# Kernel optimization log

Measured on AMD Instinct MI355X. Metric: run time of the kernel, lower is better.

Reference implementation:

```python
import jax, jax.numpy as jnp
import numpy as np

N = 50000
E = 800000
H = 2          # heads
C = 64         # out channels per head (embedding_size)
NEG_SLOPE = 0.2


def setup_inputs() -> dict:
    key = jax.random.key(0)
    ks = jax.random.split(key, 8)
    x = jax.random.normal(ks[0], (N, 1), dtype=jnp.float32)
    edge_index = jax.random.randint(ks[1], (2, E), 0, N, dtype=jnp.int64)
    edge_attr = jax.random.normal(ks[2], (E, 1), dtype=jnp.float32)
    # GATv2Conv params: lin_l, lin_r (with bias), lin_edge (no bias), att, out bias
    W_l = jax.random.normal(ks[3], (1, H * C), dtype=jnp.float32)
    b_l = jnp.zeros((H * C,), dtype=jnp.float32)
    W_r = jax.random.normal(ks[4], (1, H * C), dtype=jnp.float32)
    b_r = jnp.zeros((H * C,), dtype=jnp.float32)
    W_e = jax.random.normal(ks[5], (1, H * C), dtype=jnp.float32)
    att = jax.random.normal(ks[6], (H, C), dtype=jnp.float32)
    bias = jnp.zeros((H * C,), dtype=jnp.float32)
    return {"x": x, "edge_index": edge_index, "edge_attr": edge_attr,
            "W_l": W_l, "b_l": b_l, "W_r": W_r, "b_r": b_r,
            "W_e": W_e, "att": att, "bias": bias}


def reference(x, edge_index, edge_attr, W_l, b_l, W_r, b_r, W_e, att, bias):
    n = x.shape[0]
    src, dst = edge_index[0], edge_index[1]

    # add_self_loops=True with fill_value='mean': self-loop edge_attr at node i
    # is the mean of incoming edge_attr (0 if no incoming edges).
    attr_sum = jax.ops.segment_sum(edge_attr, dst, num_segments=n)      # [N,1]
    cnt = jax.ops.segment_sum(jnp.ones((src.shape[0], 1), edge_attr.dtype), dst, num_segments=n)
    loop_attr = attr_sum / jnp.maximum(cnt, 1.0)                         # [N,1]

    loop = jnp.arange(n, dtype=src.dtype)
    src_f = jnp.concatenate([src, loop])                                 # [E+N]
    dst_f = jnp.concatenate([dst, loop])
    attr_f = jnp.concatenate([edge_attr, loop_attr], axis=0)             # [E+N,1]

    x_l = (x @ W_l + b_l).reshape(n, H, C)    # source transform
    x_r = (x @ W_r + b_r).reshape(n, H, C)    # target transform
    e = (attr_f @ W_e).reshape(-1, H, C)      # edge feature embedding

    # GATv2 attention: leaky_relu(x_l[j] + x_r[i] + e) . att
    g = jax.nn.leaky_relu(x_l[src_f] + x_r[dst_f] + e, NEG_SLOPE)        # [E+N,H,C]
    logits = jnp.einsum('ehc,hc->eh', g, att)                            # [E+N,H]

    # segment softmax grouped by destination node
    mx = jax.ops.segment_max(logits, dst_f, num_segments=n)              # [N,H]
    a = jnp.exp(logits - mx[dst_f])
    den = jax.ops.segment_sum(a, dst_f, num_segments=n)                  # [N,H]
    alpha = a / den[dst_f]                                               # [E+N,H]

    # weighted scatter-add of source messages
    out = jax.ops.segment_sum(alpha[:, :, None] * x_l[src_f], dst_f, num_segments=n)  # [N,H,C]
    return out.reshape(n, H * C) + bias
```

## Files before the change

kernel.cpp:

```cpp
#include <hip/hip_runtime.h>

#define NEG 0.2f

typedef float f4v __attribute__((ext_vector_type(4)));

__device__ __forceinline__ float leaky(float v){ return fmaxf(v, NEG * v); }

__global__ void __launch_bounds__(256) k_edge(
        const int* __restrict__ src, const int* __restrict__ dst,
        const float* __restrict__ attr, const float* __restrict__ x,
        const float* __restrict__ Wl, const float* __restrict__ Wr,
        const float* __restrict__ We, const float* __restrict__ bl,
        const float* __restrict__ br, const float* __restrict__ att,
        int* __restrict__ head4, int* __restrict__ nxt,
        float4* __restrict__ payload, int E){
    const int sub = threadIdx.x & 15;
    const float4* Wl4 = (const float4*)Wl;
    const float4* Wr4 = (const float4*)Wr;
    const float4* We4 = (const float4*)We;
    const float4* bl4 = (const float4*)bl;
    const float4* br4 = (const float4*)br;
    const float4* at4 = (const float4*)att;
    const int q = sub * 2;
    float4 wl0 = Wl4[q], wl1 = Wl4[q+1];
    float4 wr0 = Wr4[q], wr1 = Wr4[q+1];
    float4 we0 = We4[q], we1 = We4[q+1];
    float4 b0  = bl4[q], b1  = bl4[q+1];
    float4 c0  = br4[q], c1  = br4[q+1];
    float4 a0  = at4[q], a1  = at4[q+1];
    b0.x += c0.x; b0.y += c0.y; b0.z += c0.z; b0.w += c0.w;
    b1.x += c1.x; b1.y += c1.y; b1.z += c1.z; b1.w += c1.w;

    const int gid     = (blockIdx.x * 256 + threadIdx.x) >> 4;
    const int ngroups = (gridDim.x * 256) >> 4;

    for (int e = gid; e < E; e += ngroups){
        int s = src[e], d = dst[e];
        int prev = 0;
        if (sub == 0)
            prev = atomicExch(&head4[(d << 2) + (e & 3)], e);
        float xs = x[s], xd = x[d], a = attr[e];
        float acc;
        {
            float v0 = fmaf(xs, wl0.x, fmaf(xd, wr0.x, fmaf(a, we0.x, b0.x)));
            float v1 = fmaf(xs, wl0.y, fmaf(xd, wr0.y, fmaf(a, we0.y, b0.y)));
            float v2 = fmaf(xs, wl0.z, fmaf(xd, wr0.z, fmaf(a, we0.z, b0.z)));
            float v3 = fmaf(xs, wl0.w, fmaf(xd, wr0.w, fmaf(a, we0.w, b0.w)));
            acc  = leaky(v0) * a0.x;
            acc  = fmaf(leaky(v1), a0.y, acc);
            acc  = fmaf(leaky(v2), a0.z, acc);
            acc  = fmaf(leaky(v3), a0.w, acc);
            v0 = fmaf(xs, wl1.x, fmaf(xd, wr1.x, fmaf(a, we1.x, b1.x)));
            v1 = fmaf(xs, wl1.y, fmaf(xd, wr1.y, fmaf(a, we1.y, b1.y)));
            v2 = fmaf(xs, wl1.z, fmaf(xd, wr1.z, fmaf(a, we1.z, b1.z)));
            v3 = fmaf(xs, wl1.w, fmaf(xd, wr1.w, fmaf(a, we1.w, b1.w)));
            acc  = fmaf(leaky(v0), a1.x, acc);
            acc  = fmaf(leaky(v1), a1.y, acc);
            acc  = fmaf(leaky(v2), a1.z, acc);
            acc  = fmaf(leaky(v3), a1.w, acc);
        }
        acc += __shfl_xor(acc, 1);
        acc += __shfl_xor(acc, 2);
        acc += __shfl_xor(acc, 4);
        float other = __shfl_xor(acc, 8);
        if (sub == 0){
            f4v pv = { xs, a, acc, other };
            __builtin_nontemporal_store(pv, (f4v*)&payload[e]);
            __builtin_nontemporal_store(prev, &nxt[e]);
        }
    }
}

__global__ void __launch_bounds__(256) k_walk(
        const float* __restrict__ x,
        const int* __restrict__ head4, const int* __restrict__ nxt,
        const float4* __restrict__ payload,
        const float* __restrict__ Wl, const float* __restrict__ Wr,
        const float* __restrict__ We, const float* __restrict__ bl,
        const float* __restrict__ br, const float* __restrict__ att,
        float* __restrict__ sres, int N){
    __shared__ float4 pk[128];
    int t = threadIdx.x;
    if (t < 128)
        pk[t] = make_float4(Wl[t] + Wr[t], We[t], bl[t] + br[t], att[t]);
    __syncthreads();

    int g = blockIdx.x * 256 + t;
    int i = g >> 2, sub = g & 3;
    if (i >= N) return;

    float m0 = -3.4e38f, d0 = 0.f, n0 = 0.f;
    float m1 = -3.4e38f, d1 = 0.f, n1 = 0.f;
    float asum = 0.f;
    int deg = 0;
    for (int e = head4[(i << 2) + sub]; e >= 0; e = nxt[e]){
        float4 v = payload[e];
        ++deg;
        asum += v.y;
        float mn0 = fmaxf(m0, v.z);
        float s0 = __expf(m0 - mn0), p0 = __expf(v.z - mn0);
        d0 = fmaf(d0, s0, p0);
        n0 = fmaf(n0, s0, p0 * v.x);
        m0 = mn0;
        float mn1 = fmaxf(m1, v.w);
        float s1 = __expf(m1 - mn1), p1 = __expf(v.w - mn1);
        d1 = fmaf(d1, s1, p1);
        n1 = fmaf(n1, s1, p1 * v.x);
        m1 = mn1;
    }
    #pragma unroll
    for (int off = 1; off < 4; off <<= 1){
        float om0 = __shfl_xor(m0, off), od0 = __shfl_xor(d0, off), on0 = __shfl_xor(n0, off);
        float om1 = __shfl_xor(m1, off), od1 = __shfl_xor(d1, off), on1 = __shfl_xor(n1, off);
        asum += __shfl_xor(asum, off);
        deg  += __shfl_xor(deg, off);
        float mn = fmaxf(m0, om0);
        d0 = d0 * __expf(m0 - mn) + od0 * __expf(om0 - mn);
        n0 = n0 * __expf(m0 - mn) + on0 * __expf(om0 - mn);
        m0 = mn;
        mn = fmaxf(m1, om1);
        d1 = d1 * __expf(m1 - mn) + od1 * __expf(om1 - mn);
        n1 = n1 * __expf(m1 - mn) + on1 * __expf(om1 - mn);
        m1 = mn;
    }
    float xi = x[i];
    float la = asum / (float)max(deg, 1);
    float pl = 0.f;
    #pragma unroll 8
    for (int k = 0; k < 32; ++k){
        float4 p = pk[sub * 32 + k];
        float v = fmaf(xi, p.x, fmaf(la, p.y, p.z));
        pl = fmaf(leaky(v), p.w, pl);
    }
    pl += __shfl_xor(pl, 1);
    int lane = threadIdx.x & 63;
    int base = lane & ~3;
    float l0 = __shfl(pl, base);
    float l1 = __shfl(pl, base + 2);
    if (sub == 0){
        float mn = fmaxf(m0, l0);
        float s = __expf(m0 - mn), p = __expf(l0 - mn);
        d0 = fmaf(d0, s, p);
        n0 = fmaf(n0, s, p * xi);
        mn = fmaxf(m1, l1);
        s = __expf(m1 - mn); p = __expf(l1 - mn);
        d1 = fmaf(d1, s, p);
        n1 = fmaf(n1, s, p * xi);
        sres[2 * i]     = n0 / d0;
        sres[2 * i + 1] = n1 / d1;
    }
}

__global__ void __launch_bounds__(256) k_final4(
        const float* __restrict__ sres,
        const float* __restrict__ Wl, const float* __restrict__ bl,
        const float* __restrict__ bias,
        float4* __restrict__ out, int total4){
    int t = blockIdx.x * 256 + threadIdx.x;
    if (t >= total4) return;
    int i = t >> 5;
    int q = t & 31;
    int h = q >> 4;
    float s = sres[2 * i + h];
    float4 wv = ((const float4*)Wl)[q];
    float4 bv = ((const float4*)bl)[q];
    float4 zv = ((const float4*)bias)[q];
    out[t] = make_float4(fmaf(s, wv.x, bv.x + zv.x), fmaf(s, wv.y, bv.y + zv.y),
                         fmaf(s, wv.z, bv.z + zv.z), fmaf(s, wv.w, bv.w + zv.w));
}

extern "C" void kernel_launch(void* const* d_in, const int* in_sizes, int n_in,
                              void* d_out, int out_size, void* d_ws, size_t ws_size,
                              hipStream_t stream) {
    const float* x    = (const float*)d_in[0];
    const int*   ei   = (const int*)  d_in[1];
    const float* attr = (const float*)d_in[2];
    const float* Wl   = (const float*)d_in[3];
    const float* bl   = (const float*)d_in[4];
    const float* Wr   = (const float*)d_in[5];
    const float* br   = (const float*)d_in[6];
    const float* We   = (const float*)d_in[7];
    const float* att  = (const float*)d_in[8];
    const float* bias = (const float*)d_in[9];
    float* out = (float*)d_out;

    const int N = in_sizes[0];
    const int E = in_sizes[2];
    const int* src = ei;
    const int* dst = ei + E;

    char* w = (char*)d_ws;
    float4* payload = (float4*)w;
    int*    nxt     = (int*)(w + (size_t)E * 16);
    int*    head4   = nxt + E;
    float*  sres    = (float*)(head4 + 4 * (size_t)N);

    hipMemsetAsync(head4, 0xFF, (size_t)4 * N * sizeof(int), stream);

    k_edge<<<2048, 256, 0, stream>>>(src, dst, attr, x,
                                     Wl, Wr, We, bl, br, att,
                                     head4, nxt, payload, E);
    k_walk<<<(4 * N + 255) / 256, 256, 0, stream>>>(x, head4, nxt, payload,
                                                    Wl, Wr, We, bl, br, att,
                                                    sres, N);
    k_final4<<<((size_t)N * 32 + 255) / 256, 256, 0, stream>>>(sres, Wl, bl, bias,
                                                               (float4*)out, N * 32);
}
```

Measured before the change: 86.22 us.

## Shard linked-list heads per XCC, fuse final output into walk kernel

Edge linked-list heads are split into 16 lists per node, keyed by XCC id and edge parity. The atomic exchange is relaxed to workgroup scope on the assumption that each XCC's L2 keeps its own lists coherent. The walk kernel now gives each node 16 threads, one per list, and merges the online-softmax state with 16-wide shuffles. It computes the self-loop logit in registers and writes the final output directly, which removes the k_final4 launch and the sres round trip. The costs are a 4x larger head memset, shorter parallel chain walks with more shuffle work, and a correctness risk if a workgroup-scope atomic is not coherent across the CUs of an XCC.

```diff
diff --git a/kernel.cpp b/kernel.cpp
--- a/kernel.cpp
+++ b/kernel.cpp
@@ -5,6 +5,12 @@
 typedef float f4v __attribute__((ext_vector_type(4)));
 
 __device__ __forceinline__ float leaky(float v){ return fmaxf(v, NEG * v); }
+
+__device__ __forceinline__ int xcc_id(){
+    int x;
+    asm volatile("s_getreg_b32 %0, hwreg(HW_REG_XCC_ID)" : "=s"(x));
+    return x & 7;
+}
 
 __global__ void __launch_bounds__(256) k_edge(
         const int* __restrict__ src, const int* __restrict__ dst,
@@ -12,8 +18,8 @@
         const float* __restrict__ Wl, const float* __restrict__ Wr,
         const float* __restrict__ We, const float* __restrict__ bl,
         const float* __restrict__ br, const float* __restrict__ att,
-        int* __restrict__ head4, int* __restrict__ nxt,
-        float4* __restrict__ payload, int E){
+        int* __restrict__ head, int* __restrict__ nxt,
+        float4* __restrict__ payload, int E, int N){
     const int sub = threadIdx.x & 15;
     const float4* Wl4 = (const float4*)Wl;
     const float4* Wr4 = (const float4*)Wr;
@@ -31,14 +37,19 @@
     b0.x += c0.x; b0.y += c0.y; b0.z += c0.z; b0.w += c0.w;
     b1.x += c1.x; b1.y += c1.y; b1.z += c1.z; b1.w += c1.w;
 
+    const int xcc = xcc_id();
     const int gid     = (blockIdx.x * 256 + threadIdx.x) >> 4;
     const int ngroups = (gridDim.x * 256) >> 4;
 
     for (int e = gid; e < E; e += ngroups){
         int s = src[e], d = dst[e];
         int prev = 0;
-        if (sub == 0)
-            prev = atomicExch(&head4[(d << 2) + (e & 3)], e);
+        if (sub == 0){
+            size_t hidx = (size_t)((xcc << 1) | (e & 1)) * N + d;
+            prev = __hip_atomic_exchange(&head[hidx], e,
+                                         __ATOMIC_RELAXED,
+                                         __HIP_MEMORY_SCOPE_WORKGROUP);
+        }
         float xs = x[s], xd = x[d], a = attr[e];
         float acc;
         {
@@ -73,27 +84,40 @@
 
 __global__ void __launch_bounds__(256) k_walk(
         const float* __restrict__ x,
-        const int* __restrict__ head4, const int* __restrict__ nxt,
+        const int* __restrict__ head, const int* __restrict__ nxt,
         const float4* __restrict__ payload,
         const float* __restrict__ Wl, const float* __restrict__ Wr,
         const float* __restrict__ We, const float* __restrict__ bl,
         const float* __restrict__ br, const float* __restrict__ att,
-        float* __restrict__ sres, int N){
-    __shared__ float4 pk[128];
-    int t = threadIdx.x;
-    if (t < 128)
-        pk[t] = make_float4(Wl[t] + Wr[t], We[t], bl[t] + br[t], att[t]);
-    __syncthreads();
-
-    int g = blockIdx.x * 256 + t;
-    int i = g >> 2, sub = g & 3;
+        const float* __restrict__ bias,
+        float4* __restrict__ out, int N){
+    int t = blockIdx.x * 256 + threadIdx.x;
+    int i = t >> 4, ln = t & 15;
     if (i >= N) return;
+
+    const float4* Wl4 = (const float4*)Wl;
+    const float4* Wr4 = (const float4*)Wr;
+    const float4* We4 = (const float4*)We;
+    const float4* bl4 = (const float4*)bl;
+    const float4* br4 = (const float4*)br;
+    const float4* at4 = (const float4*)att;
+    const int q = ln * 2;
+    float4 wl0 = Wl4[q], wl1 = Wl4[q+1];
+    float4 wr0 = Wr4[q], wr1 = Wr4[q+1];
+    float4 we0 = We4[q], we1 = We4[q+1];
+    float4 b0  = bl4[q], b1  = bl4[q+1];
+    float4 c0  = br4[q], c1  = br4[q+1];
+    float4 a0  = at4[q], a1  = at4[q+1];
+    wl0.x += wr0.x; wl0.y += wr0.y; wl0.z += wr0.z; wl0.w += wr0.w;
+    wl1.x += wr1.x; wl1.y += wr1.y; wl1.z += wr1.z; wl1.w += wr1.w;
+    b0.x += c0.x; b0.y += c0.y; b0.z += c0.z; b0.w += c0.w;
+    b1.x += c1.x; b1.y += c1.y; b1.z += c1.z; b1.w += c1.w;
 
     float m0 = -3.4e38f, d0 = 0.f, n0 = 0.f;
     float m1 = -3.4e38f, d1 = 0.f, n1 = 0.f;
     float asum = 0.f;
     int deg = 0;
-    for (int e = head4[(i << 2) + sub]; e >= 0; e = nxt[e]){
+    for (int e = head[(size_t)ln * N + i]; e >= 0; e = nxt[e]){
         float4 v = payload[e];
         ++deg;
         asum += v.y;
@@ -109,7 +133,7 @@
         m1 = mn1;
     }
     #pragma unroll
-    for (int off = 1; off < 4; off <<= 1){
+    for (int off = 1; off < 16; off <<= 1){
         float om0 = __shfl_xor(m0, off), od0 = __shfl_xor(d0, off), on0 = __shfl_xor(n0, off);
         float om1 = __shfl_xor(m1, off), od1 = __shfl_xor(d1, off), on1 = __shfl_xor(n1, off);
         asum += __shfl_xor(asum, off);
@@ -125,48 +149,59 @@
     }
     float xi = x[i];
     float la = asum / (float)max(deg, 1);
-    float pl = 0.f;
-    #pragma unroll 8
-    for (int k = 0; k < 32; ++k){
-        float4 p = pk[sub * 32 + k];
-        float v = fmaf(xi, p.x, fmaf(la, p.y, p.z));
-        pl = fmaf(leaky(v), p.w, pl);
+    float pl;
+    {
+        float v0 = fmaf(xi, wl0.x, fmaf(la, we0.x, b0.x));
+        float v1 = fmaf(xi, wl0.y, fmaf(la, we0.y, b0.y));
+        float v2 = fmaf(xi, wl0.z, fmaf(la, we0.z, b0.z));
+        float v3 = fmaf(xi, wl0.w, fmaf(la, we0.w, b0.w));
+        pl  = leaky(v0) * a0.x;
+        pl  = fmaf(leaky(v1), a0.y, pl);
+        pl  = fmaf(leaky(v2), a0.z, pl);
+        pl  = fmaf(leaky(v3), a0.w, pl);
+        v0 = fmaf(xi, wl1.x, fmaf(la, we1.x, b1.x));
+        v1 = fmaf(xi, wl1.y, fmaf(la, we1.y, b1.y));
+        v2 = fmaf(xi, wl1.z, fmaf(la, we1.z, b1.z));
+        v3 = fmaf(xi, wl1.w, fmaf(la, we1.w, b1.w));
+        pl  = fmaf(leaky(v0), a1.x, pl);
+        pl  = fmaf(leaky(v1), a1.y, pl);
+        pl  = fmaf(leaky(v2), a1.z, pl);
+        pl  = fmaf(leaky(v3), a1.w, pl);
     }
     pl += __shfl_xor(pl, 1);
-    int lane = threadIdx.x & 63;
-    int base = lane & ~3;
-    float l0 = __shfl(pl, base);
-    float l1 = __shfl(pl, base + 2);
-    if (sub == 0){
+    pl += __shfl_xor(pl, 2);
+    pl += __shfl_xor(pl, 4);
+    float other = __shfl_xor(pl, 8);
+    float l0 = (ln < 8) ? pl : other;
+    float l1 = (ln < 8) ? other : pl;
+    {
         float mn = fmaxf(m0, l0);
         float s = __expf(m0 - mn), p = __expf(l0 - mn);
         d0 = fmaf(d0, s, p);
         n0 = fmaf(n0, s, p * xi);
-        mn = fmaxf(m1, l1);
-        s = __expf(m1 - mn); p = __expf(l1 - mn);
+    }
+    {
+        float mn = fmaxf(m1, l1);
+        float s = __expf(m1 - mn), p = __expf(l1 - mn);
         d1 = fmaf(d1, s, p);
         n1 = fmaf(n1, s, p * xi);
-        sres[2 * i]     = n0 / d0;
-        sres[2 * i + 1] = n1 / d1;
-    }
-}
-
-__global__ void __launch_bounds__(256) k_final4(
-        const float* __restrict__ sres,
-        const float* __restrict__ Wl, const float* __restrict__ bl,
-        const float* __restrict__ bias,
-        float4* __restrict__ out, int total4){
-    int t = blockIdx.x * 256 + threadIdx.x;
-    if (t >= total4) return;
-    int i = t >> 5;
-    int q = t & 31;
-    int h = q >> 4;
-    float s = sres[2 * i + h];
-    float4 wv = ((const float4*)Wl)[q];
-    float4 bv = ((const float4*)bl)[q];
-    float4 zv = ((const float4*)bias)[q];
-    out[t] = make_float4(fmaf(s, wv.x, bv.x + zv.x), fmaf(s, wv.y, bv.y + zv.y),
-                         fmaf(s, wv.z, bv.z + zv.z), fmaf(s, wv.w, bv.w + zv.w));
+    }
+    float sres0 = n0 / d0;
+    float sres1 = n1 / d1;
+
+    const float* bs = bias;
+    float4 w0 = Wl4[ln],      w1 = Wl4[ln + 16];
+    float4 g0 = bl4[ln],      g1 = bl4[ln + 16];
+    float4 z0 = ((const float4*)bs)[ln], z1 = ((const float4*)bs)[ln + 16];
+    float4* orow = out + (size_t)i * 32;
+    orow[ln]      = make_float4(fmaf(sres0, w0.x, g0.x + z0.x),
+                                fmaf(sres0, w0.y, g0.y + z0.y),
+                                fmaf(sres0, w0.z, g0.z + z0.z),
+                                fmaf(sres0, w0.w, g0.w + z0.w));
+    orow[ln + 16] = make_float4(fmaf(sres1, w1.x, g1.x + z1.x),
+                                fmaf(sres1, w1.y, g1.y + z1.y),
+                                fmaf(sres1, w1.z, g1.z + z1.z),
+                                fmaf(sres1, w1.w, g1.w + z1.w));
 }
 
 extern "C" void kernel_launch(void* const* d_in, const int* in_sizes, int n_in,
@@ -192,17 +227,14 @@
     char* w = (char*)d_ws;
     float4* payload = (float4*)w;
     int*    nxt     = (int*)(w + (size_t)E * 16);
-    int*    head4   = nxt + E;
-    float*  sres    = (float*)(head4 + 4 * (size_t)N);
-
-    hipMemsetAsync(head4, 0xFF, (size_t)4 * N * sizeof(int), stream);
+    int*    head    = nxt + E;
+
+    hipMemsetAsync(head, 0xFF, (size_t)16 * N * sizeof(int), stream);
 
     k_edge<<<2048, 256, 0, stream>>>(src, dst, attr, x,
                                      Wl, Wr, We, bl, br, att,
-                                     head4, nxt, payload, E);
-    k_walk<<<(4 * N + 255) / 256, 256, 0, stream>>>(x, head4, nxt, payload,
-                                                    Wl, Wr, We, bl, br, att,
-                                                    sres, N);
-    k_final4<<<((size_t)N * 32 + 255) / 256, 256, 0, stream>>>(sres, Wl, bl, bias,
-                                                               (float4*)out, N * 32);
-}
+                                     head, nxt, payload, E, N);
+    k_walk<<<(16 * N + 255) / 256, 256, 0, stream>>>(x, head, nxt, payload,
+                                                     Wl, Wr, We, bl, br, att, bias,
+                                                     (float4*)out, N);
+}
```

New measurement: 79.51 us. 1.08x faster.
